# Performance work log

Measured on AMD Instinct MI355X. Metric: run time of the kernel, lower is better.

## Reference

```python
import jax, jax.numpy as jnp
import numpy as np

GRID_MIN = -2.0
GRID_MAX = 2.0
NUM_GRIDS = 8
IN_DIM = 512
OUT_DIM = 512
N = 16384
SPLINE_SCALE = 0.1


def setup_inputs() -> dict:
    key = jax.random.key(0)
    k_x, k_sw, k_w, k_b = jax.random.split(key, 4)
    x = jax.random.normal(k_x, (N, IN_DIM), dtype=jnp.float32)
    grid = jnp.linspace(GRID_MIN, GRID_MAX, NUM_GRIDS, dtype=jnp.float32)
    spline_weight = jax.random.normal(k_sw, (IN_DIM * NUM_GRIDS, OUT_DIM), dtype=jnp.float32) * SPLINE_SCALE
    bound = 1.0 / np.sqrt(IN_DIM)
    base_w = jax.random.uniform(k_w, (OUT_DIM, IN_DIM), minval=-bound, maxval=bound, dtype=jnp.float32)
    base_b = jax.random.uniform(k_b, (OUT_DIM,), minval=-bound, maxval=bound, dtype=jnp.float32)
    return {"x": x, "grid": grid, "spline_weight": spline_weight, "base_w": base_w, "base_b": base_b}


def reference(x, grid, spline_weight, base_w, base_b):
    # Gaussian RBF basis over the grid: (N, in_dim, num_grids)
    h = (GRID_MAX - GRID_MIN) / (NUM_GRIDS - 1)  # grid spacing
    basis = jnp.exp(-(((x[..., None] - grid) / h) ** 2))
    ret = basis.reshape(x.shape[0], -1) @ spline_weight  # (N, out_dim)
    base = jax.nn.silu(x) @ base_w.T + base_b
    return ret + base
```

## Files before the change

### kernel.cpp

```cpp
#include <hip/hip_runtime.h>
#include <hip/hip_bf16.h>

typedef __attribute__((ext_vector_type(8))) short short8;
typedef __attribute__((ext_vector_type(4))) float floatx4;

#define N_ROWS   16384
#define IN_DIM   512
#define OUT_DIM  512
#define K_SPLINE 4096
#define K_TOT    4608
#define BM       64
#define BN       256
#define BK       64
#define NKT      (K_TOT / BK)
#define NKTILE   (K_TOT / 32)
#define L2E      1.4426950408889634f
#define C2E      0.13533528323661270f

__device__ __forceinline__ unsigned short f2bf(float f) {
    unsigned int u = __float_as_uint(f);
    unsigned int r = u + 0x7FFFu + ((u >> 16) & 1u);
    return (unsigned short)(r >> 16);
}

__device__ __forceinline__ unsigned pack2bf(float f0, float f1) {
    unsigned u0 = __float_as_uint(f0) + 0x8000u;
    unsigned u1 = __float_as_uint(f1) + 0x8000u;
    return __builtin_amdgcn_perm(u1, u0, 0x07060302);
}

__global__ __launch_bounds__(256) void prep_kernel(
    const float* __restrict__ sw, const float* __restrict__ bw,
    unsigned short* __restrict__ Btf)
{
    const int t     = threadIdx.x;
    const int lane  = t & 63;
    const int ktile = blockIdx.x * 4 + (t >> 6);
    const int ct    = blockIdx.y;
    const int mn    = lane & 15, q = lane >> 4;
    const int n     = ct * 16 + mn;
    const int kbase = ktile * 32 + q * 8;
    short8 v;
    if (kbase < K_SPLINE) {
        #pragma unroll
        for (int j = 0; j < 8; ++j)
            v[j] = (short)f2bf(sw[(size_t)(kbase + j) * OUT_DIM + n]);
    } else {
        #pragma unroll
        for (int j = 0; j < 8; ++j)
            v[j] = (short)f2bf(bw[(size_t)n * IN_DIM + (kbase + j - K_SPLINE)]);
    }
    reinterpret_cast<short8*>(Btf)[(size_t)(ct * NKTILE + ktile) * 64 + lane] = v;
}

__device__ __forceinline__ void stageA(unsigned short* dst, const float* xrow,
                                       int rowA, int colq, int kt)
{
    unsigned short* arow = dst + rowA * 64;
    if (kt < K_SPLINE / BK) {
        const float2 xv = *reinterpret_cast<const float2*>(xrow + kt * 8 + colq * 2);
        #pragma unroll
        for (int e = 0; e < 2; ++e) {
            const float X = e ? xv.y : xv.x;
            const float u = fmaf(1.75f, X, 3.5f);
            float b = __builtin_amdgcn_exp2f(-(u * u) * L2E);
            float r = __builtin_amdgcn_exp2f(fmaf(2.0f * L2E, u, -L2E));
            float v[8];
            v[0] = b;
            #pragma unroll
            for (int j = 1; j < 8; ++j) { b *= r; r *= C2E; v[j] = b; }
            uint4 p;
            p.x = pack2bf(v[0], v[1]);
            p.y = pack2bf(v[2], v[3]);
            p.z = pack2bf(v[4], v[5]);
            p.w = pack2bf(v[6], v[7]);
            const int blk = (colq * 2 + e) ^ (rowA & 7);
            *reinterpret_cast<uint4*>(arow + blk * 8) = p;
        }
    } else {
        const float* xs = xrow + (kt - K_SPLINE / BK) * 64 + colq * 16;
        const float4 a0 = *reinterpret_cast<const float4*>(xs);
        const float4 a1 = *reinterpret_cast<const float4*>(xs + 4);
        const float4 a2 = *reinterpret_cast<const float4*>(xs + 8);
        const float4 a3 = *reinterpret_cast<const float4*>(xs + 12);
        const float f[16] = {a0.x, a0.y, a0.z, a0.w, a1.x, a1.y, a1.z, a1.w,
                             a2.x, a2.y, a2.z, a2.w, a3.x, a3.y, a3.z, a3.w};
        float s[16];
        #pragma unroll
        for (int j = 0; j < 16; ++j)
            s[j] = f[j] * __builtin_amdgcn_rcpf(
                1.0f + __builtin_amdgcn_exp2f(-f[j] * L2E));
        #pragma unroll
        for (int e = 0; e < 2; ++e) {
            uint4 p;
            p.x = pack2bf(s[e * 8 + 0], s[e * 8 + 1]);
            p.y = pack2bf(s[e * 8 + 2], s[e * 8 + 3]);
            p.z = pack2bf(s[e * 8 + 4], s[e * 8 + 5]);
            p.w = pack2bf(s[e * 8 + 6], s[e * 8 + 7]);
            const int blk = (colq * 2 + e) ^ (rowA & 7);
            *reinterpret_cast<uint4*>(arow + blk * 8) = p;
        }
    }
}

template<bool PREP>
__device__ __forceinline__ void load_bfrags(short8 dst[4][2], const short8* __restrict__ Bf,
                                            const size_t* bbase, int kt,
                                            const float* __restrict__ sw,
                                            const float* __restrict__ bw,
                                            int col0, int wn, int lane)
{
    if (PREP) {
        #pragma unroll
        for (int nt = 0; nt < 4; ++nt)
            #pragma unroll
            for (int s = 0; s < 2; ++s)
                dst[nt][s] = Bf[bbase[nt] + (size_t)(kt * 2 + s) * 64];
    } else {
        const int mn = lane & 15, q = lane >> 4;
        #pragma unroll
        for (int nt = 0; nt < 4; ++nt) {
            const int n = col0 + wn * 64 + nt * 16 + mn;
            #pragma unroll
            for (int s = 0; s < 2; ++s) {
                short8 v;
                #pragma unroll
                for (int j = 0; j < 8; ++j) {
                    const int k = (kt * 2 + s) * 32 + q * 8 + j;
                    const float val = (k < K_SPLINE)
                        ? sw[(size_t)k * OUT_DIM + n]
                        : bw[(size_t)n * IN_DIM + (k - K_SPLINE)];
                    v[j] = (short)f2bf(val);
                }
                dst[nt][s] = v;
            }
        }
    }
}

template<bool PREP>
__global__ __launch_bounds__(256, 2) void kan_kernel(
    const float* __restrict__ x,
    const unsigned short* __restrict__ Btf,
    const float* __restrict__ sw,
    const float* __restrict__ bw,
    const float* __restrict__ bias,
    float* __restrict__ out)
{
    __shared__ unsigned short Als[2][BM * BK];

    const int tid  = threadIdx.x;
    const int wn   = tid >> 6;
    const int lane = tid & 63;
    const int q    = lane >> 4;
    const int mn   = lane & 15;
    const int row0 = blockIdx.x * BM;
    const int col0 = blockIdx.y * BN;
    const int rowA = tid >> 2;
    const int colq = tid & 3;

    const float* xrow = x + (size_t)(row0 + rowA) * IN_DIM;

    size_t bbase[4];
    #pragma unroll
    for (int nt = 0; nt < 4; ++nt)
        bbase[nt] = (size_t)(((col0 >> 4) + wn * 4 + nt) * NKTILE) * 64 + lane;
    const short8* Bf = reinterpret_cast<const short8*>(Btf);

    floatx4 acc[4][4];
    #pragma unroll
    for (int i = 0; i < 4; ++i)
        #pragma unroll
        for (int j = 0; j < 4; ++j)
            acc[i][j] = (floatx4){0.f, 0.f, 0.f, 0.f};

    short8 bb[2][4][2];

    stageA(&Als[0][0], xrow, rowA, colq, 0);
    load_bfrags<PREP>(bb[0], Bf, bbase, 0, sw, bw, col0, wn, lane);
    __syncthreads();

    for (int ktb = 0; ktb < NKT; ktb += 2) {
        #pragma unroll
        for (int half = 0; half < 2; ++half) {
            const int kt  = ktb + half;
            const int cur = half;
            const int nxt = half ^ 1;
            if (kt + 1 < NKT) {
                load_bfrags<PREP>(bb[nxt], Bf, bbase, kt + 1, sw, bw, col0, wn, lane);
                stageA(&Als[nxt][0], xrow, rowA, colq, kt + 1);
            }
            #pragma unroll
            for (int s = 0; s < 2; ++s) {
                short8 af[4];
                #pragma unroll
                for (int mt = 0; mt < 4; ++mt) {
                    const int r = mt * 16 + mn;
                    af[mt] = *reinterpret_cast<const short8*>(
                        &Als[cur][r * 64 + (((s * 4 + q) ^ (r & 7)) * 8)]);
                }
                #pragma unroll
                for (int mt = 0; mt < 4; ++mt)
                    #pragma unroll
                    for (int nt = 0; nt < 4; ++nt)
                        acc[mt][nt] = __builtin_amdgcn_mfma_f32_16x16x32_bf16(
                            af[mt], bb[cur][nt][s], acc[mt][nt], 0, 0, 0);
            }
            __syncthreads();
        }
    }

    #pragma unroll
    for (int nt = 0; nt < 4; ++nt) {
        const int col = col0 + wn * 64 + nt * 16 + mn;
        const float bv = bias[col];
        #pragma unroll
        for (int mt = 0; mt < 4; ++mt) {
            const int rb = row0 + mt * 16 + q * 4;
            #pragma unroll
            for (int e = 0; e < 4; ++e)
                out[(size_t)(rb + e) * OUT_DIM + col] = acc[mt][nt][e] + bv;
        }
    }
}

extern "C" void kernel_launch(void* const* d_in, const int* in_sizes, int n_in,
                              void* d_out, int out_size, void* d_ws, size_t ws_size,
                              hipStream_t stream)
{
    const float* x    = (const float*)d_in[0];
    const float* sw   = (const float*)d_in[2];
    const float* bw   = (const float*)d_in[3];
    const float* bias = (const float*)d_in[4];
    float* out = (float*)d_out;

    const size_t bt_bytes = (size_t)OUT_DIM * K_TOT * sizeof(unsigned short);
    if (ws_size >= bt_bytes) {
        unsigned short* Btf = (unsigned short*)d_ws;
        prep_kernel<<<dim3(NKTILE / 4, OUT_DIM / 16), 256, 0, stream>>>(sw, bw, Btf);
        kan_kernel<true><<<dim3(N_ROWS / BM, OUT_DIM / BN), 256, 0, stream>>>(
            x, Btf, sw, bw, bias, out);
    } else {
        kan_kernel<false><<<dim3(N_ROWS / BM, OUT_DIM / BN), 256, 0, stream>>>(
            x, nullptr, sw, bw, bias, out);
    }
}
```

Before: 174.4 us.

## Widen A-stage to 128-K per barrier with register-prefetched x and split B loads

Each shared-memory A stage now holds 128 K-columns instead of 64, so each pair of MFMA sub-steps needs only one barrier instead of two. The x values for the next spline stage are prefetched into registers one step ahead. B fragments are loaded in two halves interleaved with the MFMA work, and the swizzle is widened to 16 blocks to match the larger tile. The block index is flattened so the two column halves of the same row tile run as adjacent blocks, which should help L2 reuse of x. bf16 packing switches from round-to-nearest to truncation, which trades a little accuracy for fewer ALU ops. LDS use doubles, which could affect occupancy.

```diff
diff --git a/kernel.cpp b/kernel.cpp
--- a/kernel.cpp
+++ b/kernel.cpp
@@ -9,11 +9,10 @@
 #define OUT_DIM  512
 #define K_SPLINE 4096
 #define K_TOT    4608
-#define BM       64
-#define BN       256
-#define BK       64
-#define NKT      (K_TOT / BK)
-#define NKTILE   (K_TOT / 32)
+#define NKT      72
+#define NPER     36
+#define NSPER    32
+#define NKTILE   144
 #define L2E      1.4426950408889634f
 #define C2E      0.13533528323661270f
 
@@ -23,10 +22,8 @@
     return (unsigned short)(r >> 16);
 }
 
-__device__ __forceinline__ unsigned pack2bf(float f0, float f1) {
-    unsigned u0 = __float_as_uint(f0) + 0x8000u;
-    unsigned u1 = __float_as_uint(f1) + 0x8000u;
-    return __builtin_amdgcn_perm(u1, u0, 0x07060302);
+__device__ __forceinline__ unsigned packtrunc(float f0, float f1) {
+    return __builtin_amdgcn_perm(__float_as_uint(f1), __float_as_uint(f0), 0x07060302);
 }
 
 __global__ __launch_bounds__(256) void prep_kernel(
@@ -35,11 +32,11 @@
 {
     const int t     = threadIdx.x;
     const int lane  = t & 63;
-    const int ktile = blockIdx.x * 4 + (t >> 6);
+    const int kt32  = blockIdx.x * 4 + (t >> 6);
     const int ct    = blockIdx.y;
     const int mn    = lane & 15, q = lane >> 4;
     const int n     = ct * 16 + mn;
-    const int kbase = ktile * 32 + q * 8;
+    const int kbase = kt32 * 32 + q * 8;
     short8 v;
     if (kbase < K_SPLINE) {
         #pragma unroll
@@ -50,55 +47,56 @@
         for (int j = 0; j < 8; ++j)
             v[j] = (short)f2bf(bw[(size_t)n * IN_DIM + (kbase + j - K_SPLINE)]);
     }
-    reinterpret_cast<short8*>(Btf)[(size_t)(ct * NKTILE + ktile) * 64 + lane] = v;
-}
-
-__device__ __forceinline__ void stageA(unsigned short* dst, const float* xrow,
-                                       int rowA, int colq, int kt)
-{
-    unsigned short* arow = dst + rowA * 64;
-    if (kt < K_SPLINE / BK) {
-        const float2 xv = *reinterpret_cast<const float2*>(xrow + kt * 8 + colq * 2);
-        #pragma unroll
-        for (int e = 0; e < 2; ++e) {
-            const float X = e ? xv.y : xv.x;
-            const float u = fmaf(1.75f, X, 3.5f);
-            float b = __builtin_amdgcn_exp2f(-(u * u) * L2E);
-            float r = __builtin_amdgcn_exp2f(fmaf(2.0f * L2E, u, -L2E));
-            float v[8];
-            v[0] = b;
-            #pragma unroll
-            for (int j = 1; j < 8; ++j) { b *= r; r *= C2E; v[j] = b; }
-            uint4 p;
-            p.x = pack2bf(v[0], v[1]);
-            p.y = pack2bf(v[2], v[3]);
-            p.z = pack2bf(v[4], v[5]);
-            p.w = pack2bf(v[6], v[7]);
-            const int blk = (colq * 2 + e) ^ (rowA & 7);
-            *reinterpret_cast<uint4*>(arow + blk * 8) = p;
-        }
-    } else {
-        const float* xs = xrow + (kt - K_SPLINE / BK) * 64 + colq * 16;
-        const float4 a0 = *reinterpret_cast<const float4*>(xs);
-        const float4 a1 = *reinterpret_cast<const float4*>(xs + 4);
-        const float4 a2 = *reinterpret_cast<const float4*>(xs + 8);
-        const float4 a3 = *reinterpret_cast<const float4*>(xs + 12);
-        const float f[16] = {a0.x, a0.y, a0.z, a0.w, a1.x, a1.y, a1.z, a1.w,
-                             a2.x, a2.y, a2.z, a2.w, a3.x, a3.y, a3.z, a3.w};
-        float s[16];
-        #pragma unroll
-        for (int j = 0; j < 16; ++j)
-            s[j] = f[j] * __builtin_amdgcn_rcpf(
-                1.0f + __builtin_amdgcn_exp2f(-f[j] * L2E));
-        #pragma unroll
-        for (int e = 0; e < 2; ++e) {
-            uint4 p;
-            p.x = pack2bf(s[e * 8 + 0], s[e * 8 + 1]);
-            p.y = pack2bf(s[e * 8 + 2], s[e * 8 + 3]);
-            p.z = pack2bf(s[e * 8 + 4], s[e * 8 + 5]);
-            p.w = pack2bf(s[e * 8 + 6], s[e * 8 + 7]);
-            const int blk = (colq * 2 + e) ^ (rowA & 7);
-            *reinterpret_cast<uint4*>(arow + blk * 8) = p;
+    reinterpret_cast<short8*>(Btf)[(size_t)(ct * NKTILE + kt32) * 64 + lane] = v;
+}
+
+__device__ __forceinline__ uint4 basis_pack(float X) {
+    const float u = fmaf(1.75f, X, 3.5f);
+    float b = __builtin_amdgcn_exp2f(-(u * u) * L2E);
+    float r = __builtin_amdgcn_exp2f(fmaf(2.0f * L2E, u, -L2E));
+    float v[8];
+    v[0] = b;
+    #pragma unroll
+    for (int j = 1; j < 8; ++j) { b *= r; r *= C2E; v[j] = b; }
+    uint4 p;
+    p.x = packtrunc(v[0], v[1]);
+    p.y = packtrunc(v[2], v[3]);
+    p.z = packtrunc(v[4], v[5]);
+    p.w = packtrunc(v[6], v[7]);
+    return p;
+}
+
+__device__ __forceinline__ void stageA128(unsigned short* dst, const float* xrow,
+                                          int rowA, int colq, int p, float4 xsp)
+{
+    unsigned short* arow = dst + rowA * 128;
+    if (p < NSPER) {
+        const float xv[4] = {xsp.x, xsp.y, xsp.z, xsp.w};
+        #pragma unroll
+        for (int e = 0; e < 4; ++e) {
+            const uint4 pk = basis_pack(xv[e]);
+            const int blk = (colq * 4 + e) ^ (rowA & 15);
+            *reinterpret_cast<uint4*>(arow + blk * 8) = pk;
+        }
+    } else {
+        const float* xs = xrow + (p - NSPER) * 128 + colq * 32;
+        #pragma unroll
+        for (int e = 0; e < 4; ++e) {
+            const float4 a0 = *reinterpret_cast<const float4*>(xs + e * 8);
+            const float4 a1 = *reinterpret_cast<const float4*>(xs + e * 8 + 4);
+            const float f[8] = {a0.x, a0.y, a0.z, a0.w, a1.x, a1.y, a1.z, a1.w};
+            float s[8];
+            #pragma unroll
+            for (int j = 0; j < 8; ++j)
+                s[j] = f[j] * __builtin_amdgcn_rcpf(
+                    1.0f + __builtin_amdgcn_exp2f(-f[j] * L2E));
+            uint4 pk;
+            pk.x = packtrunc(s[0], s[1]);
+            pk.y = packtrunc(s[2], s[3]);
+            pk.z = packtrunc(s[4], s[5]);
+            pk.w = packtrunc(s[6], s[7]);
+            const int blk = (colq * 4 + e) ^ (rowA & 15);
+            *reinterpret_cast<uint4*>(arow + blk * 8) = pk;
         }
     }
 }
@@ -108,8 +106,9 @@
                                             const size_t* bbase, int kt,
                                             const float* __restrict__ sw,
                                             const float* __restrict__ bw,
-                                            int col0, int wn, int lane)
-{
+                                            int col0, int lane)
+{
+    if (kt >= NKT) return;
     if (PREP) {
         #pragma unroll
         for (int nt = 0; nt < 4; ++nt)
@@ -120,7 +119,7 @@
         const int mn = lane & 15, q = lane >> 4;
         #pragma unroll
         for (int nt = 0; nt < 4; ++nt) {
-            const int n = col0 + wn * 64 + nt * 16 + mn;
+            const int n = col0 + nt * 16 + mn;
             #pragma unroll
             for (int s = 0; s < 2; ++s) {
                 short8 v;
@@ -147,24 +146,25 @@
     const float* __restrict__ bias,
     float* __restrict__ out)
 {
-    __shared__ unsigned short Als[2][BM * BK];
+    __shared__ unsigned short Als[2][64 * 128];
 
     const int tid  = threadIdx.x;
     const int wn   = tid >> 6;
     const int lane = tid & 63;
     const int q    = lane >> 4;
     const int mn   = lane & 15;
-    const int row0 = blockIdx.x * BM;
-    const int col0 = blockIdx.y * BN;
+    const int bid  = blockIdx.x;
+    const int row0 = (bid >> 1) * 64;
+    const int col0 = (bid & 1) * 256 + wn * 64;
+
     const int rowA = tid >> 2;
     const int colq = tid & 3;
-
     const float* xrow = x + (size_t)(row0 + rowA) * IN_DIM;
 
     size_t bbase[4];
     #pragma unroll
     for (int nt = 0; nt < 4; ++nt)
-        bbase[nt] = (size_t)(((col0 >> 4) + wn * 4 + nt) * NKTILE) * 64 + lane;
+        bbase[nt] = (size_t)(((col0 >> 4) + nt) * NKTILE) * 64 + lane;
     const short8* Bf = reinterpret_cast<const short8*>(Btf);
 
     floatx4 acc[4][4];
@@ -176,43 +176,53 @@
 
     short8 bb[2][4][2];
 
-    stageA(&Als[0][0], xrow, rowA, colq, 0);
-    load_bfrags<PREP>(bb[0], Bf, bbase, 0, sw, bw, col0, wn, lane);
+    float4 xsp = *reinterpret_cast<const float4*>(xrow + colq * 4);
+    stageA128(&Als[0][0], xrow, rowA, colq, 0, xsp);
+    load_bfrags<PREP>(bb[0], Bf, bbase, 0, sw, bw, col0, lane);
+    xsp = *reinterpret_cast<const float4*>(xrow + 16 + colq * 4);
     __syncthreads();
 
-    for (int ktb = 0; ktb < NKT; ktb += 2) {
-        #pragma unroll
-        for (int half = 0; half < 2; ++half) {
-            const int kt  = ktb + half;
-            const int cur = half;
-            const int nxt = half ^ 1;
-            if (kt + 1 < NKT) {
-                load_bfrags<PREP>(bb[nxt], Bf, bbase, kt + 1, sw, bw, col0, wn, lane);
-                stageA(&Als[nxt][0], xrow, rowA, colq, kt + 1);
-            }
+    for (int p = 0; p < NPER; ++p) {
+        const unsigned short* Acur = &Als[p & 1][0];
+        unsigned short*       Anxt = &Als[(p & 1) ^ 1][0];
+
+        load_bfrags<PREP>(bb[1], Bf, bbase, 2 * p + 1, sw, bw, col0, lane);
+
+        if (p + 1 < NPER) {
+            stageA128(Anxt, xrow, rowA, colq, p + 1, xsp);
+            if (p + 2 < NSPER)
+                xsp = *reinterpret_cast<const float4*>(
+                    xrow + (p + 2) * 16 + colq * 4);
+        }
+
+        #pragma unroll
+        for (int hh = 0; hh < 2; ++hh) {
             #pragma unroll
             for (int s = 0; s < 2; ++s) {
+                const int st = hh * 2 + s;
                 short8 af[4];
                 #pragma unroll
                 for (int mt = 0; mt < 4; ++mt) {
                     const int r = mt * 16 + mn;
                     af[mt] = *reinterpret_cast<const short8*>(
-                        &Als[cur][r * 64 + (((s * 4 + q) ^ (r & 7)) * 8)]);
+                        Acur + r * 128 + (((st * 4 + q) ^ (r & 15)) * 8));
                 }
                 #pragma unroll
                 for (int mt = 0; mt < 4; ++mt)
                     #pragma unroll
                     for (int nt = 0; nt < 4; ++nt)
                         acc[mt][nt] = __builtin_amdgcn_mfma_f32_16x16x32_bf16(
-                            af[mt], bb[cur][nt][s], acc[mt][nt], 0, 0, 0);
+                            af[mt], bb[hh][nt][s], acc[mt][nt], 0, 0, 0);
             }
-            __syncthreads();
-        }
+            if (hh == 0)
+                load_bfrags<PREP>(bb[0], Bf, bbase, 2 * p + 2, sw, bw, col0, lane);
+        }
+        __syncthreads();
     }
 
     #pragma unroll
     for (int nt = 0; nt < 4; ++nt) {
-        const int col = col0 + wn * 64 + nt * 16 + mn;
+        const int col = col0 + nt * 16 + mn;
         const float bv = bias[col];
         #pragma unroll
         for (int mt = 0; mt < 4; ++mt) {
@@ -238,10 +248,10 @@
     if (ws_size >= bt_bytes) {
         unsigned short* Btf = (unsigned short*)d_ws;
         prep_kernel<<<dim3(NKTILE / 4, OUT_DIM / 16), 256, 0, stream>>>(sw, bw, Btf);
-        kan_kernel<true><<<dim3(N_ROWS / BM, OUT_DIM / BN), 256, 0, stream>>>(
+        kan_kernel<true><<<dim3(512), 256, 0, stream>>>(
             x, Btf, sw, bw, bias, out);
     } else {
-        kan_kernel<false><<<dim3(N_ROWS / BM, OUT_DIM / BN), 256, 0, stream>>>(
+        kan_kernel<false><<<dim3(512), 256, 0, stream>>>(
             x, nullptr, sw, bw, bias, out);
     }
 }
```

New measurement: 167.5 us. 3.9% less time.
